# Kernel tuning notes

Hardware: AMD Instinct MI355X
Metric: run time of the kernel (lower is better)

## Reference

```python
import jax, jax.numpy as jnp
import numpy as np


def setup_inputs() -> dict:
    key = jax.random.key(0)
    kq, kk, kv = jax.random.split(key, 3)
    B, H, S, D = 2, 16, 2048, 64
    return {
        "queries": jax.random.normal(kq, (B, H, S, D), dtype=jnp.float32),
        "keys": jax.random.normal(kk, (B, H, S, D), dtype=jnp.float32),
        "values": jax.random.normal(kv, (B, H, S, D), dtype=jnp.float32),
        "d_k": D,
    }


def reference(queries, keys, values, d_k):
    # scores = Q K^T / sqrt(d_k)  -> [B, H, S, S]
    scale = 1.0 / jnp.sqrt(jnp.asarray(d_k, dtype=queries.dtype))
    scores = jnp.einsum("bhqd,bhkd->bhqk", queries, keys) * scale
    weights = jax.nn.softmax(scores, axis=-1)
    return jnp.einsum("bhqk,bhkd->bhqd", weights, values)
```

## Files before the change

kernel.cpp:

```cpp
#include <hip/hip_runtime.h>


typedef _Float16 half8 __attribute__((ext_vector_type(8)));
typedef _Float16 half4 __attribute__((ext_vector_type(4)));
typedef __fp16 fp16x2 __attribute__((ext_vector_type(2)));
typedef float floatx4 __attribute__((ext_vector_type(4)));

constexpr int BQ = 128;
constexpr int BK = 64;
constexpr int DH = 64;
constexpr int SLEN = 2048;
constexpr int NT = SLEN / BK;
constexpr int THREADS = 256;

#define MFMA16(a, b, c) __builtin_amdgcn_mfma_f32_16x16x32_f16(a, b, c, 0, 0, 0)

#define fast_exp2 __builtin_amdgcn_exp2f

static __device__ __forceinline__ void load_lds16(const _Float16* g, _Float16* l) {
    __builtin_amdgcn_global_load_lds(
        (const __attribute__((address_space(1))) void*)g,
        (__attribute__((address_space(3))) void*)l, 16, 0, 0);
}

__global__ __launch_bounds__(256)
void prep_frags(const float* __restrict__ K, const float* __restrict__ V,
                _Float16* __restrict__ F)
{
    __shared__ _Float16 kt_[64 * 72];
    __shared__ _Float16 vt_[64 * 72];
    const int tid  = threadIdx.x;
    const int tile = blockIdx.x & 31;
    const int head = blockIdx.x >> 5;
    const size_t base = ((size_t)head * SLEN + tile * 64) * DH;
    const float4* Ks = (const float4*)(K + base);
    const float4* Vs = (const float4*)(V + base);
    #pragma unroll
    for (int r = 0; r < 4; r++) {
        int i = tid + 256 * r, row = i >> 4, g = i & 15;
        float4 a = Ks[row * 16 + g];
        half4 h;
        h[0] = (_Float16)a.x; h[1] = (_Float16)a.y;
        h[2] = (_Float16)a.z; h[3] = (_Float16)a.w;
        *(half4*)&kt_[row * 72 + g * 4] = h;
        float4 b = Vs[row * 16 + g];
        half4 h2;
        h2[0] = (_Float16)b.x; h2[1] = (_Float16)b.y;
        h2[2] = (_Float16)b.z; h2[3] = (_Float16)b.w;
        *(half4*)&vt_[row * 72 + g * 4] = h2;
    }
    __syncthreads();
    _Float16* dst = F + (size_t)(head * 32 + tile) * 8192;
    #pragma unroll
    for (int r = 0; r < 2; r++) {
        int s = tid + 256 * r;
        int frag = s >> 6, lane = s & 63;
        int kd = frag >> 2, c = frag & 3;
        int quad = lane >> 4, n16 = lane & 15;
        int key = (c >> 1) * 32 + (c & 1) * 4 + (n16 >> 2) * 8 + (n16 & 3);
        *(half8*)&dst[s * 8] = *(const half8*)&kt_[key * 72 + kd * 32 + quad * 8];
    }
    #pragma unroll
    for (int r = 0; r < 2; r++) {
        int s = tid + 256 * r;
        int frag = s >> 6, lane = s & 63;
        int kd2 = frag >> 2, c2 = frag & 3;
        int quad = lane >> 4, n16 = lane & 15;
        int d = c2 * 16 + n16;
        int key0 = kd2 * 32 + quad * 8;
        half8 h;
        #pragma unroll
        for (int j = 0; j < 8; j++) h[j] = vt_[(key0 + j) * 72 + d];
        *(half8*)&dst[4096 + s * 8] = h;
    }
}

__global__ __launch_bounds__(THREADS, 2)
void attn_f16_mfma(const float* __restrict__ Q, const _Float16* __restrict__ F,
                   float* __restrict__ Out, const int* __restrict__ dkp)
{
    __shared__ _Float16 lds[2][8192];

    const int tid  = threadIdx.x;
    const int wq   = tid >> 6;
    const int lane = tid & 63;
    const int quad = lane >> 4;
    const int n16  = lane & 15;

    const int id   = blockIdx.x;
    const int xcd  = id & 7;
    const int slot = id >> 3;
    const int head = xcd * 4 + (slot >> 4);
    const int qt   = slot & 15;

    const float scale2 = rsqrtf((float)(*dkp)) * 1.44269504088896340736f;
    const size_t headoff = (size_t)head * SLEN * DH;

    half8 qB[2][2];
    {
        const float4* Qg = (const float4*)(Q + headoff + (size_t)(qt * BQ + wq * 32) * DH);
        #pragma unroll
        for (int rg = 0; rg < 2; rg++)
            #pragma unroll
            for (int kd = 0; kd < 2; kd++) {
                int row = rg * 16 + n16;
                float4 a = Qg[row * 16 + kd * 8 + quad * 2];
                float4 b = Qg[row * 16 + kd * 8 + quad * 2 + 1];
                half8 h;
                h[0] = (_Float16)(a.x * scale2); h[1] = (_Float16)(a.y * scale2);
                h[2] = (_Float16)(a.z * scale2); h[3] = (_Float16)(a.w * scale2);
                h[4] = (_Float16)(b.x * scale2); h[5] = (_Float16)(b.y * scale2);
                h[6] = (_Float16)(b.z * scale2); h[7] = (_Float16)(b.w * scale2);
                qB[rg][kd] = h;
            }
    }

    const _Float16* Fh = F + (size_t)head * 32 * 8192;

    auto stage = [&](_Float16* dst, int kt) {
        const _Float16* src = Fh + (size_t)kt * 8192 + wq * 512 + lane * 8;
        #pragma unroll
        for (int i = 0; i < 4; i++)
            load_lds16(src + i * 2048, dst + wq * 512 + i * 2048);
    };

    floatx4 oacc[2][4];
    floatx4 lsum[2];
    const floatx4 fz = {0.f, 0.f, 0.f, 0.f};
    #pragma unroll
    for (int rg = 0; rg < 2; rg++) {
        lsum[rg] = fz;
        #pragma unroll
        for (int c2 = 0; c2 < 4; c2++) oacc[rg][c2] = fz;
    }
    half8 ones;
    #pragma unroll
    for (int j = 0; j < 8; j++) ones[j] = (_Float16)1.0f;

    union PU { fp16x2 h2[4]; half8 h8; };

    auto tile_compute = [&](const _Float16* Bl) {
        const _Float16* Kl = Bl;
        const _Float16* Vl = Bl + 4096;

        half8 kA[2][4];
        #pragma unroll
        for (int kd = 0; kd < 2; kd++)
            #pragma unroll
            for (int c = 0; c < 4; c++)
                kA[kd][c] = *(const half8*)&Kl[((kd * 4 + c) * 64 + lane) * 8];

        floatx4 sC[2][4];
        #pragma unroll
        for (int rg = 0; rg < 2; rg++)
            #pragma unroll
            for (int c = 0; c < 4; c++) {
                floatx4 acc = MFMA16(kA[0][c], qB[rg][0], fz);
                sC[rg][c] = MFMA16(kA[1][c], qB[rg][1], acc);
            }

        half8 pB[2][2];
        #pragma unroll
        for (int rg = 0; rg < 2; rg++)
            #pragma unroll
            for (int kd2 = 0; kd2 < 2; kd2++) {
                PU u_;
                u_.h2[0] = __builtin_amdgcn_cvt_pkrtz(fast_exp2(sC[rg][kd2 * 2][0]),
                                                      fast_exp2(sC[rg][kd2 * 2][1]));
                u_.h2[1] = __builtin_amdgcn_cvt_pkrtz(fast_exp2(sC[rg][kd2 * 2][2]),
                                                      fast_exp2(sC[rg][kd2 * 2][3]));
                u_.h2[2] = __builtin_amdgcn_cvt_pkrtz(fast_exp2(sC[rg][kd2 * 2 + 1][0]),
                                                      fast_exp2(sC[rg][kd2 * 2 + 1][1]));
                u_.h2[3] = __builtin_amdgcn_cvt_pkrtz(fast_exp2(sC[rg][kd2 * 2 + 1][2]),
                                                      fast_exp2(sC[rg][kd2 * 2 + 1][3]));
                pB[rg][kd2] = u_.h8;
            }

        half8 vA[2][4];
        #pragma unroll
        for (int kd2 = 0; kd2 < 2; kd2++)
            #pragma unroll
            for (int c2 = 0; c2 < 4; c2++)
                vA[kd2][c2] = *(const half8*)&Vl[((kd2 * 4 + c2) * 64 + lane) * 8];

        __builtin_amdgcn_s_setprio(1);
        #pragma unroll
        for (int rg = 0; rg < 2; rg++) {
            lsum[rg] = MFMA16(ones, pB[rg][0], lsum[rg]);
            lsum[rg] = MFMA16(ones, pB[rg][1], lsum[rg]);
        }
        #pragma unroll
        for (int rg = 0; rg < 2; rg++)
            #pragma unroll
            for (int c2 = 0; c2 < 4; c2++) {
                oacc[rg][c2] = MFMA16(vA[0][c2], pB[rg][0], oacc[rg][c2]);
                oacc[rg][c2] = MFMA16(vA[1][c2], pB[rg][1], oacc[rg][c2]);
            }
        __builtin_amdgcn_s_setprio(0);
    };

    stage(&lds[0][0], 0);

    for (int kt = 0; kt < NT; kt += 2) {
        asm volatile("s_waitcnt vmcnt(0)" ::: "memory");
        __builtin_amdgcn_sched_barrier(0);
        __syncthreads();
        if (kt + 1 < NT) stage(&lds[1][0], kt + 1);
        tile_compute(&lds[0][0]);

        asm volatile("s_waitcnt vmcnt(0)" ::: "memory");
        __builtin_amdgcn_sched_barrier(0);
        __syncthreads();
        if (kt + 2 < NT) stage(&lds[0][0], kt + 2);
        tile_compute(&lds[1][0]);
    }

    float* Og = Out + headoff + (size_t)(qt * BQ + wq * 32) * DH;
    #pragma unroll
    for (int rg = 0; rg < 2; rg++) {
        float inv = 1.0f / lsum[rg][0];
        #pragma unroll
        for (int c2 = 0; c2 < 4; c2++) {
            floatx4 v = oacc[rg][c2];
            float4 w = make_float4(v[0] * inv, v[1] * inv, v[2] * inv, v[3] * inv);
            *(float4*)&Og[(rg * 16 + n16) * DH + c2 * 16 + quad * 4] = w;
        }
    }
}

extern "C" void kernel_launch(void* const* d_in, const int* in_sizes, int n_in,
                              void* d_out, int out_size, void* d_ws, size_t ws_size,
                              hipStream_t stream) {
    const float* Q = (const float*)d_in[0];
    const float* K = (const float*)d_in[1];
    const float* V = (const float*)d_in[2];
    const int*  dk = (const int*)d_in[3];
    float* Out = (float*)d_out;

    const int nbh = in_sizes[0] / (SLEN * DH);

    _Float16* F = (_Float16*)d_ws;

    prep_frags<<<nbh * 32, 256, 0, stream>>>(K, V, F);

    dim3 grid(nbh * (SLEN / BQ));
    attn_f16_mfma<<<grid, THREADS, 0, stream>>>(Q, F, Out, dk);
}
```

Before: 133.4 us.

## Software-pipeline PV MFMAs of previous tile with QK and exp of current tile

Restructures the key-tile loop so that each window loads K and V fragments for the current tile, issues the PV and row-sum MFMAs for the previous tile, then computes QK scores and exp2 for the current tile. The aim is to overlap the exp/convert ALU work with independent matrix-core work instead of serializing score, softmax and PV within one tile. It holds double sets of P and V fragments in registers, which raises register pressure at two waves per SIMD and risks spills or lower occupancy. It also adds a prologue and epilogue to drain the pipeline.

```diff
diff --git a/kernel.cpp b/kernel.cpp
--- a/kernel.cpp
+++ b/kernel.cpp
@@ -139,81 +139,80 @@
 
     union PU { fp16x2 h2[4]; half8 h8; };
 
-    auto tile_compute = [&](const _Float16* Bl) {
-        const _Float16* Kl = Bl;
-        const _Float16* Vl = Bl + 4096;
-
-        half8 kA[2][4];
-        #pragma unroll
-        for (int kd = 0; kd < 2; kd++)
-            #pragma unroll
-            for (int c = 0; c < 4; c++)
-                kA[kd][c] = *(const half8*)&Kl[((kd * 4 + c) * 64 + lane) * 8];
-
-        floatx4 sC[2][4];
-        #pragma unroll
-        for (int rg = 0; rg < 2; rg++)
-            #pragma unroll
-            for (int c = 0; c < 4; c++) {
-                floatx4 acc = MFMA16(kA[0][c], qB[rg][0], fz);
-                sC[rg][c] = MFMA16(kA[1][c], qB[rg][1], acc);
-            }
-
-        half8 pB[2][2];
-        #pragma unroll
-        for (int rg = 0; rg < 2; rg++)
-            #pragma unroll
-            for (int kd2 = 0; kd2 < 2; kd2++) {
-                PU u_;
-                u_.h2[0] = __builtin_amdgcn_cvt_pkrtz(fast_exp2(sC[rg][kd2 * 2][0]),
-                                                      fast_exp2(sC[rg][kd2 * 2][1]));
-                u_.h2[1] = __builtin_amdgcn_cvt_pkrtz(fast_exp2(sC[rg][kd2 * 2][2]),
-                                                      fast_exp2(sC[rg][kd2 * 2][3]));
-                u_.h2[2] = __builtin_amdgcn_cvt_pkrtz(fast_exp2(sC[rg][kd2 * 2 + 1][0]),
-                                                      fast_exp2(sC[rg][kd2 * 2 + 1][1]));
-                u_.h2[3] = __builtin_amdgcn_cvt_pkrtz(fast_exp2(sC[rg][kd2 * 2 + 1][2]),
-                                                      fast_exp2(sC[rg][kd2 * 2 + 1][3]));
-                pB[rg][kd2] = u_.h8;
-            }
-
-        half8 vA[2][4];
-        #pragma unroll
-        for (int kd2 = 0; kd2 < 2; kd2++)
-            #pragma unroll
-            for (int c2 = 0; c2 < 4; c2++)
-                vA[kd2][c2] = *(const half8*)&Vl[((kd2 * 4 + c2) * 64 + lane) * 8];
-
-        __builtin_amdgcn_s_setprio(1);
-        #pragma unroll
-        for (int rg = 0; rg < 2; rg++) {
-            lsum[rg] = MFMA16(ones, pB[rg][0], lsum[rg]);
-            lsum[rg] = MFMA16(ones, pB[rg][1], lsum[rg]);
+    half8 pB0[2][2], pB1[2][2], vA0[2][4], vA1[2][4];
+
+#define WINDOW(Bl, PBP, VAP, PBN, VAN, DOPREV, SDST, ST, DOSTAGE) do {         \
+    asm volatile("s_waitcnt vmcnt(0)" ::: "memory");                           \
+    __builtin_amdgcn_sched_barrier(0);                                         \
+    __syncthreads();                                                           \
+    if (DOSTAGE) stage(SDST, ST);                                              \
+    const _Float16* Kl_ = (Bl);                                                \
+    const _Float16* Vl_ = (Bl) + 4096;                                         \
+    half8 kA_[2][4];                                                           \
+    _Pragma("unroll") for (int kd = 0; kd < 2; kd++)                           \
+    _Pragma("unroll") for (int c = 0; c < 4; c++)                              \
+        kA_[kd][c] = *(const half8*)&Kl_[((kd * 4 + c) * 64 + lane) * 8];      \
+    _Pragma("unroll") for (int kd2 = 0; kd2 < 2; kd2++)                        \
+    _Pragma("unroll") for (int c2 = 0; c2 < 4; c2++)                           \
+        VAN[kd2][c2] = *(const half8*)&Vl_[((kd2 * 4 + c2) * 64 + lane) * 8];  \
+    if (DOPREV) {                                                              \
+        __builtin_amdgcn_s_setprio(1);                                         \
+        _Pragma("unroll") for (int rg = 0; rg < 2; rg++) {                     \
+            lsum[rg] = MFMA16(ones, PBP[rg][0], lsum[rg]);                     \
+            lsum[rg] = MFMA16(ones, PBP[rg][1], lsum[rg]);                     \
+        }                                                                      \
+        _Pragma("unroll") for (int rg = 0; rg < 2; rg++)                       \
+        _Pragma("unroll") for (int c2 = 0; c2 < 4; c2++) {                     \
+            oacc[rg][c2] = MFMA16(VAP[0][c2], PBP[rg][0], oacc[rg][c2]);       \
+            oacc[rg][c2] = MFMA16(VAP[1][c2], PBP[rg][1], oacc[rg][c2]);       \
+        }                                                                      \
+        __builtin_amdgcn_s_setprio(0);                                         \
+    }                                                                          \
+    floatx4 sC_[2][4];                                                         \
+    _Pragma("unroll") for (int rg = 0; rg < 2; rg++)                           \
+    _Pragma("unroll") for (int c = 0; c < 4; c++) {                            \
+        floatx4 acc_ = MFMA16(kA_[0][c], qB[rg][0], fz);                       \
+        sC_[rg][c] = MFMA16(kA_[1][c], qB[rg][1], acc_);                       \
+    }                                                                          \
+    _Pragma("unroll") for (int rg = 0; rg < 2; rg++)                           \
+    _Pragma("unroll") for (int kd2 = 0; kd2 < 2; kd2++) {                      \
+        PU u_;                                                                 \
+        u_.h2[0] = __builtin_amdgcn_cvt_pkrtz(fast_exp2(sC_[rg][kd2 * 2][0]),  \
+                                              fast_exp2(sC_[rg][kd2 * 2][1])); \
+        u_.h2[1] = __builtin_amdgcn_cvt_pkrtz(fast_exp2(sC_[rg][kd2 * 2][2]),  \
+                                              fast_exp2(sC_[rg][kd2 * 2][3])); \
+        u_.h2[2] = __builtin_amdgcn_cvt_pkrtz(fast_exp2(sC_[rg][kd2 * 2 + 1][0]), \
+                                              fast_exp2(sC_[rg][kd2 * 2 + 1][1])); \
+        u_.h2[3] = __builtin_amdgcn_cvt_pkrtz(fast_exp2(sC_[rg][kd2 * 2 + 1][2]), \
+                                              fast_exp2(sC_[rg][kd2 * 2 + 1][3])); \
+        PBN[rg][kd2] = u_.h8;                                                  \
+    }                                                                          \
+} while (0)
+
+    stage(&lds[0][0], 0);
+
+    WINDOW(&lds[0][0], pB1, vA1, pB0, vA0, false, &lds[1][0], 1, true);
+
+    for (int kt = 1; kt < NT - 1; kt += 2) {
+        WINDOW(&lds[1][0], pB0, vA0, pB1, vA1, true, &lds[0][0], kt + 1, true);
+        WINDOW(&lds[0][0], pB1, vA1, pB0, vA0, true, &lds[1][0], kt + 2,
+               (kt + 2 < NT));
+    }
+
+    WINDOW(&lds[1][0], pB0, vA0, pB1, vA1, true, &lds[0][0], 0, false);
+
+    #pragma unroll
+    for (int rg = 0; rg < 2; rg++) {
+        lsum[rg] = MFMA16(ones, pB1[rg][0], lsum[rg]);
+        lsum[rg] = MFMA16(ones, pB1[rg][1], lsum[rg]);
+    }
+    #pragma unroll
+    for (int rg = 0; rg < 2; rg++)
+        #pragma unroll
+        for (int c2 = 0; c2 < 4; c2++) {
+            oacc[rg][c2] = MFMA16(vA1[0][c2], pB1[rg][0], oacc[rg][c2]);
+            oacc[rg][c2] = MFMA16(vA1[1][c2], pB1[rg][1], oacc[rg][c2]);
         }
-        #pragma unroll
-        for (int rg = 0; rg < 2; rg++)
-            #pragma unroll
-            for (int c2 = 0; c2 < 4; c2++) {
-                oacc[rg][c2] = MFMA16(vA[0][c2], pB[rg][0], oacc[rg][c2]);
-                oacc[rg][c2] = MFMA16(vA[1][c2], pB[rg][1], oacc[rg][c2]);
-            }
-        __builtin_amdgcn_s_setprio(0);
-    };
-
-    stage(&lds[0][0], 0);
-
-    for (int kt = 0; kt < NT; kt += 2) {
-        asm volatile("s_waitcnt vmcnt(0)" ::: "memory");
-        __builtin_amdgcn_sched_barrier(0);
-        __syncthreads();
-        if (kt + 1 < NT) stage(&lds[1][0], kt + 1);
-        tile_compute(&lds[0][0]);
-
-        asm volatile("s_waitcnt vmcnt(0)" ::: "memory");
-        __builtin_amdgcn_sched_barrier(0);
-        __syncthreads();
-        if (kt + 2 < NT) stage(&lds[0][0], kt + 2);
-        tile_compute(&lds[1][0]);
-    }
 
     float* Og = Out + headoff + (size_t)(qt * BQ + wq * 32) * DH;
     #pragma unroll
```

Result: faster. 129.4 us (-3.0%).

## Fuse K/V fp16 conversion into attention kernel via register-staged prefetch

Applied to the files above, without the earlier changes.

Removes the separate prep kernel that converted K and V to fp16 fragment layout in a workspace. The attention kernel now loads fp32 K and V tiles straight into registers, overlaps those loads with compute on the current tile, then converts and writes them to LDS in fragment order. This saves a kernel launch and a workspace round trip. The cost is that every query-tile block rereads fp32 K/V, doubling the bytes loaded. The V reads are strided scalar loads, and the extra registers may reduce occupancy.

```diff
diff --git a/kernel.cpp b/kernel.cpp
--- a/kernel.cpp
+++ b/kernel.cpp
@@ -2,7 +2,6 @@
 
 
 typedef _Float16 half8 __attribute__((ext_vector_type(8)));
-typedef _Float16 half4 __attribute__((ext_vector_type(4)));
 typedef __fp16 fp16x2 __attribute__((ext_vector_type(2)));
 typedef float floatx4 __attribute__((ext_vector_type(4)));
 
@@ -17,67 +16,10 @@
 
 #define fast_exp2 __builtin_amdgcn_exp2f
 
-static __device__ __forceinline__ void load_lds16(const _Float16* g, _Float16* l) {
-    __builtin_amdgcn_global_load_lds(
-        (const __attribute__((address_space(1))) void*)g,
-        (__attribute__((address_space(3))) void*)l, 16, 0, 0);
-}
-
-__global__ __launch_bounds__(256)
-void prep_frags(const float* __restrict__ K, const float* __restrict__ V,
-                _Float16* __restrict__ F)
-{
-    __shared__ _Float16 kt_[64 * 72];
-    __shared__ _Float16 vt_[64 * 72];
-    const int tid  = threadIdx.x;
-    const int tile = blockIdx.x & 31;
-    const int head = blockIdx.x >> 5;
-    const size_t base = ((size_t)head * SLEN + tile * 64) * DH;
-    const float4* Ks = (const float4*)(K + base);
-    const float4* Vs = (const float4*)(V + base);
-    #pragma unroll
-    for (int r = 0; r < 4; r++) {
-        int i = tid + 256 * r, row = i >> 4, g = i & 15;
-        float4 a = Ks[row * 16 + g];
-        half4 h;
-        h[0] = (_Float16)a.x; h[1] = (_Float16)a.y;
-        h[2] = (_Float16)a.z; h[3] = (_Float16)a.w;
-        *(half4*)&kt_[row * 72 + g * 4] = h;
-        float4 b = Vs[row * 16 + g];
-        half4 h2;
-        h2[0] = (_Float16)b.x; h2[1] = (_Float16)b.y;
-        h2[2] = (_Float16)b.z; h2[3] = (_Float16)b.w;
-        *(half4*)&vt_[row * 72 + g * 4] = h2;
-    }
-    __syncthreads();
-    _Float16* dst = F + (size_t)(head * 32 + tile) * 8192;
-    #pragma unroll
-    for (int r = 0; r < 2; r++) {
-        int s = tid + 256 * r;
-        int frag = s >> 6, lane = s & 63;
-        int kd = frag >> 2, c = frag & 3;
-        int quad = lane >> 4, n16 = lane & 15;
-        int key = (c >> 1) * 32 + (c & 1) * 4 + (n16 >> 2) * 8 + (n16 & 3);
-        *(half8*)&dst[s * 8] = *(const half8*)&kt_[key * 72 + kd * 32 + quad * 8];
-    }
-    #pragma unroll
-    for (int r = 0; r < 2; r++) {
-        int s = tid + 256 * r;
-        int frag = s >> 6, lane = s & 63;
-        int kd2 = frag >> 2, c2 = frag & 3;
-        int quad = lane >> 4, n16 = lane & 15;
-        int d = c2 * 16 + n16;
-        int key0 = kd2 * 32 + quad * 8;
-        half8 h;
-        #pragma unroll
-        for (int j = 0; j < 8; j++) h[j] = vt_[(key0 + j) * 72 + d];
-        *(half8*)&dst[4096 + s * 8] = h;
-    }
-}
-
 __global__ __launch_bounds__(THREADS, 2)
-void attn_f16_mfma(const float* __restrict__ Q, const _Float16* __restrict__ F,
-                   float* __restrict__ Out, const int* __restrict__ dkp)
+void attn_f16_mfma(const float* __restrict__ Q, const float* __restrict__ K,
+                   const float* __restrict__ V, float* __restrict__ Out,
+                   const int* __restrict__ dkp)
 {
     __shared__ _Float16 lds[2][8192];
 
@@ -115,13 +57,58 @@
             }
     }
 
-    const _Float16* Fh = F + (size_t)head * 32 * 8192;
-
-    auto stage = [&](_Float16* dst, int kt) {
-        const _Float16* src = Fh + (size_t)kt * 8192 + wq * 512 + lane * 8;
-        #pragma unroll
-        for (int i = 0; i < 4; i++)
-            load_lds16(src + i * 2048, dst + wq * 512 + i * 2048);
+    const float* Kg = K + headoff;
+    const float* Vg = V + headoff;
+
+    int koff[2], voff[2];
+    #pragma unroll
+    for (int i = 0; i < 2; i++) {
+        int s = wq * 64 + i * 256 + lane;
+        int frag = s >> 6, kd = frag >> 2, c = frag & 3;
+        int key = (c >> 1) * 32 + (c & 1) * 4 + ((lane & 15) >> 2) * 8 + (lane & 3);
+        koff[i] = key * 64 + kd * 32 + (lane >> 4) * 8;
+    }
+    #pragma unroll
+    for (int i = 0; i < 2; i++) {
+        int s = wq * 64 + i * 256 + lane;
+        int frag = s >> 6, kd2 = frag >> 2, c2 = frag & 3;
+        voff[i] = (kd2 * 32 + (lane >> 4) * 8) * 64 + c2 * 16 + (lane & 15);
+    }
+
+    float4 kreg[2][2];
+    float  vreg[2][8];
+
+    auto load_regs = [&](int kt) {
+        #pragma unroll
+        for (int i = 0; i < 2; i++) {
+            const float* p = Kg + (size_t)kt * 4096 + koff[i];
+            kreg[i][0] = *(const float4*)p;
+            kreg[i][1] = *(const float4*)(p + 4);
+        }
+        #pragma unroll
+        for (int i = 0; i < 2; i++) {
+            const float* p = Vg + (size_t)kt * 4096 + voff[i];
+            #pragma unroll
+            for (int j = 0; j < 8; j++) vreg[i][j] = p[j * 64];
+        }
+    };
+    auto write_regs = [&](_Float16* dst) {
+        #pragma unroll
+        for (int i = 0; i < 2; i++) {
+            half8 h;
+            h[0] = (_Float16)kreg[i][0].x; h[1] = (_Float16)kreg[i][0].y;
+            h[2] = (_Float16)kreg[i][0].z; h[3] = (_Float16)kreg[i][0].w;
+            h[4] = (_Float16)kreg[i][1].x; h[5] = (_Float16)kreg[i][1].y;
+            h[6] = (_Float16)kreg[i][1].z; h[7] = (_Float16)kreg[i][1].w;
+            *(half8*)&dst[(size_t)(wq * 64 + i * 256 + lane) * 8] = h;
+        }
+        #pragma unroll
+        for (int i = 0; i < 2; i++) {
+            half8 h;
+            #pragma unroll
+            for (int j = 0; j < 8; j++) h[j] = (_Float16)vreg[i][j];
+            *(half8*)&dst[(size_t)(512 + wq * 64 + i * 256 + lane) * 8] = h;
+        }
     };
 
     floatx4 oacc[2][4];
@@ -199,20 +186,21 @@
         __builtin_amdgcn_s_setprio(0);
     };
 
-    stage(&lds[0][0], 0);
+    load_regs(0);
+    write_regs(&lds[0][0]);
 
     for (int kt = 0; kt < NT; kt += 2) {
-        asm volatile("s_waitcnt vmcnt(0)" ::: "memory");
+        __syncthreads();
+        if (kt + 1 < NT) load_regs(kt + 1);
         __builtin_amdgcn_sched_barrier(0);
+        tile_compute(&lds[0][0]);
+        if (kt + 1 < NT) write_regs(&lds[1][0]);
+
         __syncthreads();
-        if (kt + 1 < NT) stage(&lds[1][0], kt + 1);
-        tile_compute(&lds[0][0]);
-
-        asm volatile("s_waitcnt vmcnt(0)" ::: "memory");
+        if (kt + 2 < NT) load_regs(kt + 2);
         __builtin_amdgcn_sched_barrier(0);
-        __syncthreads();
-        if (kt + 2 < NT) stage(&lds[0][0], kt + 2);
         tile_compute(&lds[1][0]);
+        if (kt + 2 < NT) write_regs(&lds[0][0]);
     }
 
     float* Og = Out + headoff + (size_t)(qt * BQ + wq * 32) * DH;
@@ -238,11 +226,8 @@
     float* Out = (float*)d_out;
 
     const int nbh = in_sizes[0] / (SLEN * DH);
-
-    _Float16* F = (_Float16*)d_ws;
-
-    prep_frags<<<nbh * 32, 256, 0, stream>>>(K, V, F);
+    (void)d_ws; (void)ws_size;
 
     dim3 grid(nbh * (SLEN / BQ));
-    attn_f16_mfma<<<grid, THREADS, 0, stream>>>(Q, F, Out, dk);
+    attn_f16_mfma<<<grid, THREADS, 0, stream>>>(Q, K, V, Out, dk);
 }
```

Result: faster. 128.0 us (-4.0%).
